# Performance work log

Measured on AMD Instinct MI355X. Metric: run time of the kernel, lower is better.

## Reference

```python
import math
import jax, jax.numpy as jnp
import numpy as np

IN_SIZE = 1024
OUT_SIZE = 1024
LOG_N = 10          # ceil(log2(in_size))
NSTACKS = 1         # ceil(out_size / 2**LOG_N)
NBLOCKS = 1


def setup_inputs() -> dict:
    key = jax.random.key(0)
    k1, k2, k3 = jax.random.split(key, 3)
    x = jax.random.normal(k1, (8, 4096, IN_SIZE), dtype=jnp.float32)
    # twiddle init: randn * 1/sqrt(2)  (ortho_init=False, real)
    twiddle = jax.random.normal(
        k2, (NSTACKS, NBLOCKS, LOG_N, IN_SIZE // 2, 2, 2), dtype=jnp.float32
    ) * (1.0 / math.sqrt(2.0))
    bound = 1.0 / math.sqrt(IN_SIZE)
    bias = jax.random.uniform(k3, (OUT_SIZE,), minval=-bound, maxval=bound,
                              dtype=jnp.float32)
    return {"x": x, "twiddle": twiddle, "bias": bias}


def butterfly_multiply(twiddle, x, increasing_stride=True):
    """twiddle: (nstacks, nblocks, log_n, n/2, 2, 2); x: (batch, nstacks, n)."""
    b, nstacks, n = x.shape
    nblocks, log_n = twiddle.shape[1], twiddle.shape[2]
    out = x
    inc = increasing_stride
    for blk in range(nblocks):
        for idx in range(log_n):
            log_stride = idx if inc else log_n - 1 - idx
            stride = 1 << log_stride
            # t: (nstacks, n/(2*stride), stride, 2, 2)
            t = twiddle[:, blk, idx].reshape(nstacks, n // (2 * stride), stride, 2, 2)
            # o: (batch, nstacks, n/(2*stride), 2, stride)
            o = out.reshape(b, nstacks, n // (2 * stride), 2, stride)
            # 2x2 rotation applied across pairs separated by `stride`
            out = jnp.einsum('sgrij,bsgjr->bsgir', t, o).reshape(b, nstacks, n)
        inc = not inc
    return out


def reference(x, twiddle, bias):
    batch_shape = x.shape[:-1]
    xf = x.reshape(-1, IN_SIZE)                       # pre_process (no pad: 1024=2**10)
    xb = jnp.broadcast_to(xf[:, None, :], (xf.shape[0], NSTACKS, IN_SIZE))
    out = butterfly_multiply(twiddle, xb, increasing_stride=True)
    out = out.reshape(xf.shape[0], NSTACKS * IN_SIZE)[:, :OUT_SIZE]
    out = out + bias
    return out.reshape(*batch_shape, OUT_SIZE)
```

## Files before the change

kernel.cpp:

```cpp
#include <hip/hip_runtime.h>


#define ROWS_PER_WAVE 4
#define N 1024

__global__ __launch_bounds__(256) void permute_tw_kernel(
    const float* __restrict__ tw, float* __restrict__ ws)
{
    const int s = blockIdx.x;
    const int t = threadIdx.x;
    #pragma unroll
    for (int it = 0; it < 8; ++it) {
        const int g = it * 256 + t;
        const float val = tw[s * 2048 + g];
        int dst;
        if (s < 4) {
            const int l  = g >> 5;
            const int r  = g & 31;
            dst = (r >> 2) * 256 + l * 4 + (r & 3);
        } else {
            const int p  = g >> 2;
            const int c  = g & 3;
            const int i  = c >> 1;
            const int j  = c & 1;
            const int pl = p >> 4;
            const int k  = p & 15;
            const int lm = s - 4;
            const int m  = 1 << lm;
            const int l  = ((pl >> lm) << (lm + 1)) | (i << lm) | (pl & (m - 1));
            dst = (k >> 1) * 256 + l * 4 + (k & 1) * 2 + (j ^ i);
        }
        ws[s * 2048 + dst] = val;
    }
}

__global__ __launch_bounds__(256, 4) void butterfly_kernel(
    const float* __restrict__ x,
    const float* __restrict__ ws,
    const float* __restrict__ bias,
    float* __restrict__ out,
    int nRows)
{
    const int lane = threadIdx.x & 63;
    const int waveInBlock = threadIdx.x >> 6;
    const int waveId = blockIdx.x * 4 + waveInBlock;
    const long rowBase = (long)waveId * ROWS_PER_WAVE;
    if (rowBase >= nRows) return;

    const int off = lane * 16;

    float v[ROWS_PER_WAVE][16];

    #pragma unroll
    for (int r = 0; r < ROWS_PER_WAVE; ++r) {
        const float4* p = (const float4*)(x + (rowBase + r) * N + off);
        #pragma unroll
        for (int q = 0; q < 4; ++q) {
            float4 f = p[q];
            v[r][q*4+0] = f.x; v[r][q*4+1] = f.y;
            v[r][q*4+2] = f.z; v[r][q*4+3] = f.w;
        }
    }

    #pragma unroll
    for (int stage = 0; stage < 4; ++stage) {
        const int s = 1 << stage;
        float t[32];
        const float4* tp = (const float4*)(ws + stage * 2048) + lane;
        #pragma unroll
        for (int q = 0; q < 8; ++q) {
            float4 f = tp[q * 64];
            t[q*4+0] = f.x; t[q*4+1] = f.y; t[q*4+2] = f.z; t[q*4+3] = f.w;
        }
        #pragma unroll
        for (int r = 0; r < ROWS_PER_WAVE; ++r) {
            #pragma unroll
            for (int j = 0; j < 8; ++j) {
                const int p0 = ((j >> stage) << (stage + 1)) | (j & (s - 1));
                const int p1 = p0 | s;
                float a = v[r][p0], b = v[r][p1];
                v[r][p0] = t[j*4+0] * a + t[j*4+1] * b;
                v[r][p1] = t[j*4+2] * a + t[j*4+3] * b;
            }
        }
    }

    #pragma unroll
    for (int stage = 4; stage < 10; ++stage) {
        const int m = 1 << (stage - 4);
        float ta_[16], tb_[16];
        const float4* tp = (const float4*)(ws + stage * 2048) + lane;
        #pragma unroll
        for (int kk = 0; kk < 8; ++kk) {
            float4 f = tp[kk * 64];
            ta_[2*kk+0] = f.x; tb_[2*kk+0] = f.y;
            ta_[2*kk+1] = f.z; tb_[2*kk+1] = f.w;
        }
        #pragma unroll
        for (int r = 0; r < ROWS_PER_WAVE; ++r) {
            #pragma unroll
            for (int k = 0; k < 16; ++k) {
                float mine  = v[r][k];
                float other = __shfl_xor(mine, m, 64);
                v[r][k] = ta_[k] * mine + tb_[k] * other;
            }
        }
    }

    float bv[16];
    {
        const float4* bp = (const float4*)(bias + off);
        #pragma unroll
        for (int q = 0; q < 4; ++q) {
            float4 f = bp[q];
            bv[q*4+0] = f.x; bv[q*4+1] = f.y;
            bv[q*4+2] = f.z; bv[q*4+3] = f.w;
        }
    }
    #pragma unroll
    for (int r = 0; r < ROWS_PER_WAVE; ++r) {
        float4* p = (float4*)(out + (rowBase + r) * N + off);
        #pragma unroll
        for (int q = 0; q < 4; ++q) {
            float4 f;
            f.x = v[r][q*4+0] + bv[q*4+0];
            f.y = v[r][q*4+1] + bv[q*4+1];
            f.z = v[r][q*4+2] + bv[q*4+2];
            f.w = v[r][q*4+3] + bv[q*4+3];
            p[q] = f;
        }
    }
}

extern "C" void kernel_launch(void* const* d_in, const int* in_sizes, int n_in,
                              void* d_out, int out_size, void* d_ws, size_t ws_size,
                              hipStream_t stream) {
    const float* x    = (const float*)d_in[0];
    const float* tw   = (const float*)d_in[1];
    const float* bias = (const float*)d_in[2];
    float* out = (float*)d_out;
    float* ws  = (float*)d_ws;

    permute_tw_kernel<<<10, 256, 0, stream>>>(tw, ws);

    const int nRows = in_sizes[0] / N;
    const int waves = (nRows + ROWS_PER_WAVE - 1) / ROWS_PER_WAVE;
    const int blocks = (waves + 3) / 4;

    butterfly_kernel<<<blocks, 256, 0, stream>>>(x, ws, bias, out, nRows);
}
```

Baseline: 299.5 us.

## Stage twiddles in LDS, software-pipeline row loads, use ds_swizzle for exchanges

Each block copies the permuted twiddles for nine stages into dynamic shared memory, and the last stage still reads from global memory. Each wave handles eight rows in pairs, with double-buffered register loads so the next rows' global reads overlap the current butterfly compute. Lane exchanges with xor distance below 32 use ds_swizzle instead of shfl_xor. The aim is to cut repeated global twiddle traffic and hide memory latency. The costs are a 72KB LDS footprint per block, which limits occupancy, a per-block copy cost, and the risk that twiddle reads are now bound by LDS bandwidth.

After: 880.2 us. 194% more time.

```diff
diff --git a/kernel.cpp b/kernel.cpp
--- a/kernel.cpp
+++ b/kernel.cpp
@@ -1,8 +1,11 @@
 #include <hip/hip_runtime.h>
 
 
-#define ROWS_PER_WAVE 4
 #define N 1024
+#define BLOCK_THREADS 512
+#define WAVES_PER_BLOCK 8
+#define ROWS_PER_WAVE 8
+#define LDS_STAGES 9
 
 __global__ __launch_bounds__(256) void permute_tw_kernel(
     const float* __restrict__ tw, float* __restrict__ ws)
@@ -34,101 +37,166 @@
     }
 }
 
-__global__ __launch_bounds__(256, 4) void butterfly_kernel(
+template<int M>
+__device__ __forceinline__ float sx(float v) {
+    if constexpr (M < 32) {
+        return __int_as_float(__builtin_amdgcn_ds_swizzle(
+            __float_as_int(v), (M << 10) | 0x1f));
+    } else {
+        return __shfl_xor(v, 32, 64);
+    }
+}
+
+__device__ __forceinline__ void loadRow(float (&v)[16],
+                                        const float* __restrict__ x,
+                                        long row, int off)
+{
+    const float4* p = (const float4*)(x + row * N + off);
+    #pragma unroll
+    for (int q = 0; q < 4; ++q) {
+        float4 f = p[q];
+        v[q*4+0] = f.x; v[q*4+1] = f.y;
+        v[q*4+2] = f.z; v[q*4+3] = f.w;
+    }
+}
+
+__device__ __forceinline__ void computeStore(
+    float (&v0)[16], float (&v1)[16],
+    const float* ldsTw,
+    const float* __restrict__ ws,
+    const float* __restrict__ bias,
+    float* __restrict__ out,
+    long row, int lane, int nRows)
+{
+    const int off = lane * 16;
+
+    #pragma unroll
+    for (int stage = 0; stage < 4; ++stage) {
+        const int s = 1 << stage;
+        float t[32];
+        const float4* tp = (const float4*)(ldsTw + stage * 2048) + lane;
+        #pragma unroll
+        for (int q = 0; q < 8; ++q) {
+            float4 f = tp[q * 64];
+            t[q*4+0] = f.x; t[q*4+1] = f.y; t[q*4+2] = f.z; t[q*4+3] = f.w;
+        }
+        #pragma unroll
+        for (int j = 0; j < 8; ++j) {
+            const int p0 = ((j >> stage) << (stage + 1)) | (j & (s - 1));
+            const int p1 = p0 | s;
+            { float a = v0[p0], b = v0[p1];
+              v0[p0] = t[j*4+0]*a + t[j*4+1]*b;
+              v0[p1] = t[j*4+2]*a + t[j*4+3]*b; }
+            { float a = v1[p0], b = v1[p1];
+              v1[p0] = t[j*4+0]*a + t[j*4+1]*b;
+              v1[p1] = t[j*4+2]*a + t[j*4+3]*b; }
+        }
+    }
+
+#define XSTAGE(STG, BASEPTR) { \
+    constexpr int M = 1 << ((STG) - 4); \
+    float ta_[16], tb_[16]; \
+    const float4* tp = (const float4*)((BASEPTR) + (STG) * 2048) + lane; \
+    _Pragma("unroll") \
+    for (int kk = 0; kk < 8; ++kk) { \
+        float4 f = tp[kk * 64]; \
+        ta_[2*kk+0] = f.x; tb_[2*kk+0] = f.y; \
+        ta_[2*kk+1] = f.z; tb_[2*kk+1] = f.w; } \
+    _Pragma("unroll") \
+    for (int k = 0; k < 16; ++k) { \
+        float m0 = v0[k], o0 = sx<M>(m0); \
+        float m1 = v1[k], o1 = sx<M>(m1); \
+        v0[k] = ta_[k]*m0 + tb_[k]*o0; \
+        v1[k] = ta_[k]*m1 + tb_[k]*o1; } \
+}
+    XSTAGE(4, ldsTw)
+    XSTAGE(5, ldsTw)
+    XSTAGE(6, ldsTw)
+    XSTAGE(7, ldsTw)
+    XSTAGE(8, ldsTw)
+    XSTAGE(9, ws)
+#undef XSTAGE
+
+    float bv[16];
+    {
+        const float4* bp = (const float4*)(bias + off);
+        #pragma unroll
+        for (int q = 0; q < 4; ++q) {
+            float4 f = bp[q];
+            bv[q*4+0] = f.x; bv[q*4+1] = f.y;
+            bv[q*4+2] = f.z; bv[q*4+3] = f.w;
+        }
+    }
+    if (row < nRows) {
+        float4* p = (float4*)(out + row * N + off);
+        #pragma unroll
+        for (int q = 0; q < 4; ++q) {
+            float4 f;
+            f.x = v0[q*4+0] + bv[q*4+0];
+            f.y = v0[q*4+1] + bv[q*4+1];
+            f.z = v0[q*4+2] + bv[q*4+2];
+            f.w = v0[q*4+3] + bv[q*4+3];
+            p[q] = f;
+        }
+    }
+    if (row + 1 < nRows) {
+        float4* p = (float4*)(out + (row + 1) * N + off);
+        #pragma unroll
+        for (int q = 0; q < 4; ++q) {
+            float4 f;
+            f.x = v1[q*4+0] + bv[q*4+0];
+            f.y = v1[q*4+1] + bv[q*4+1];
+            f.z = v1[q*4+2] + bv[q*4+2];
+            f.w = v1[q*4+3] + bv[q*4+3];
+            p[q] = f;
+        }
+    }
+}
+
+__global__ __launch_bounds__(BLOCK_THREADS, 4) void butterfly_kernel(
     const float* __restrict__ x,
     const float* __restrict__ ws,
     const float* __restrict__ bias,
     float* __restrict__ out,
     int nRows)
 {
+    extern __shared__ float ldsTw[];
+
+    {
+        const int t = threadIdx.x;
+        const float4* src = (const float4*)ws;
+        float4* dst = (float4*)ldsTw;
+        #pragma unroll
+        for (int i = 0; i < (LDS_STAGES * 2048 / 4) / BLOCK_THREADS; ++i)
+            dst[i * BLOCK_THREADS + t] = src[i * BLOCK_THREADS + t];
+    }
+    __syncthreads();
+
     const int lane = threadIdx.x & 63;
-    const int waveInBlock = threadIdx.x >> 6;
-    const int waveId = blockIdx.x * 4 + waveInBlock;
+    const int off = lane * 16;
+    const int waveId = blockIdx.x * WAVES_PER_BLOCK + (threadIdx.x >> 6);
     const long rowBase = (long)waveId * ROWS_PER_WAVE;
     if (rowBase >= nRows) return;
 
-    const int off = lane * 16;
-
-    float v[ROWS_PER_WAVE][16];
-
-    #pragma unroll
-    for (int r = 0; r < ROWS_PER_WAVE; ++r) {
-        const float4* p = (const float4*)(x + (rowBase + r) * N + off);
-        #pragma unroll
-        for (int q = 0; q < 4; ++q) {
-            float4 f = p[q];
-            v[r][q*4+0] = f.x; v[r][q*4+1] = f.y;
-            v[r][q*4+2] = f.z; v[r][q*4+3] = f.w;
-        }
-    }
-
-    #pragma unroll
-    for (int stage = 0; stage < 4; ++stage) {
-        const int s = 1 << stage;
-        float t[32];
-        const float4* tp = (const float4*)(ws + stage * 2048) + lane;
-        #pragma unroll
-        for (int q = 0; q < 8; ++q) {
-            float4 f = tp[q * 64];
-            t[q*4+0] = f.x; t[q*4+1] = f.y; t[q*4+2] = f.z; t[q*4+3] = f.w;
-        }
-        #pragma unroll
-        for (int r = 0; r < ROWS_PER_WAVE; ++r) {
-            #pragma unroll
-            for (int j = 0; j < 8; ++j) {
-                const int p0 = ((j >> stage) << (stage + 1)) | (j & (s - 1));
-                const int p1 = p0 | s;
-                float a = v[r][p0], b = v[r][p1];
-                v[r][p0] = t[j*4+0] * a + t[j*4+1] * b;
-                v[r][p1] = t[j*4+2] * a + t[j*4+3] * b;
-            }
-        }
-    }
-
-    #pragma unroll
-    for (int stage = 4; stage < 10; ++stage) {
-        const int m = 1 << (stage - 4);
-        float ta_[16], tb_[16];
-        const float4* tp = (const float4*)(ws + stage * 2048) + lane;
-        #pragma unroll
-        for (int kk = 0; kk < 8; ++kk) {
-            float4 f = tp[kk * 64];
-            ta_[2*kk+0] = f.x; tb_[2*kk+0] = f.y;
-            ta_[2*kk+1] = f.z; tb_[2*kk+1] = f.w;
-        }
-        #pragma unroll
-        for (int r = 0; r < ROWS_PER_WAVE; ++r) {
-            #pragma unroll
-            for (int k = 0; k < 16; ++k) {
-                float mine  = v[r][k];
-                float other = __shfl_xor(mine, m, 64);
-                v[r][k] = ta_[k] * mine + tb_[k] * other;
-            }
-        }
-    }
-
-    float bv[16];
-    {
-        const float4* bp = (const float4*)(bias + off);
-        #pragma unroll
-        for (int q = 0; q < 4; ++q) {
-            float4 f = bp[q];
-            bv[q*4+0] = f.x; bv[q*4+1] = f.y;
-            bv[q*4+2] = f.z; bv[q*4+3] = f.w;
-        }
-    }
-    #pragma unroll
-    for (int r = 0; r < ROWS_PER_WAVE; ++r) {
-        float4* p = (float4*)(out + (rowBase + r) * N + off);
-        #pragma unroll
-        for (int q = 0; q < 4; ++q) {
-            float4 f;
-            f.x = v[r][q*4+0] + bv[q*4+0];
-            f.y = v[r][q*4+1] + bv[q*4+1];
-            f.z = v[r][q*4+2] + bv[q*4+2];
-            f.w = v[r][q*4+3] + bv[q*4+3];
-            p[q] = f;
-        }
+    float A0[16], A1[16], B0[16], B1[16];
+
+    auto clampRow = [&](long r) { return r < nRows ? r : rowBase; };
+
+    loadRow(A0, x, rowBase, off);
+    loadRow(A1, x, clampRow(rowBase + 1), off);
+
+    long r = rowBase;
+    #pragma unroll 1
+    for (int it = 0; it < 2; ++it) {
+        loadRow(B0, x, clampRow(r + 2), off);
+        loadRow(B1, x, clampRow(r + 3), off);
+        computeStore(A0, A1, ldsTw, ws, bias, out, r, lane, nRows);
+        if (it == 0) {
+            loadRow(A0, x, clampRow(r + 4), off);
+            loadRow(A1, x, clampRow(r + 5), off);
+        }
+        computeStore(B0, B1, ldsTw, ws, bias, out, r + 2, lane, nRows);
+        r += 4;
     }
 }
 
@@ -141,11 +209,21 @@
     float* out = (float*)d_out;
     float* ws  = (float*)d_ws;
 
+    const size_t ldsBytes = (size_t)LDS_STAGES * 2048 * sizeof(float);
+    static bool attrSet = false;
+    if (!attrSet) {
+        hipFuncSetAttribute((const void*)butterfly_kernel,
+                            hipFuncAttributeMaxDynamicSharedMemorySize,
+                            (int)ldsBytes);
+        attrSet = true;
+    }
+
     permute_tw_kernel<<<10, 256, 0, stream>>>(tw, ws);
 
     const int nRows = in_sizes[0] / N;
-    const int waves = (nRows + ROWS_PER_WAVE - 1) / ROWS_PER_WAVE;
-    const int blocks = (waves + 3) / 4;
-
-    butterfly_kernel<<<blocks, 256, 0, stream>>>(x, ws, bias, out, nRows);
-}
+    const int rowsPerBlock = WAVES_PER_BLOCK * ROWS_PER_WAVE;
+    const int blocks = (nRows + rowsPerBlock - 1) / rowsPerBlock;
+
+    butterfly_kernel<<<blocks, BLOCK_THREADS, ldsBytes, stream>>>(
+        x, ws, bias, out, nRows);
+}
```

## Stage twiddles in LDS, use ds_swizzle for cross-lane exchanges, widen blocks

Applied to the files above, without the earlier changes.

Each block first copies all ten permuted twiddle stages (80 KB) into shared memory, and the butterfly stages then read twiddles from LDS instead of global memory. Cross-lane exchanges with xor distance below 32 now use ds_swizzle instead of the generic shuffle. Blocks grow to 512 threads so the LDS fill is shared across 8 waves. Every block now pays for an 80 KB copy plus a barrier, and the large LDS footprint limits how many blocks fit per CU, which can cut occupancy on this memory-bound kernel.

New measurement: 267.3 us. 1.12x faster.

```diff
diff --git a/kernel.cpp b/kernel.cpp
--- a/kernel.cpp
+++ b/kernel.cpp
@@ -1,8 +1,11 @@
 #include <hip/hip_runtime.h>
 
 
+#define N 1024
+#define BLOCK_THREADS 512
+#define WAVES_PER_BLOCK 8
 #define ROWS_PER_WAVE 4
-#define N 1024
+#define NSTAGES 10
 
 __global__ __launch_bounds__(256) void permute_tw_kernel(
     const float* __restrict__ tw, float* __restrict__ ws)
@@ -34,20 +37,40 @@
     }
 }
 
-__global__ __launch_bounds__(256, 4) void butterfly_kernel(
+template<int M>
+__device__ __forceinline__ float sx(float v) {
+    if constexpr (M < 32) {
+        return __int_as_float(__builtin_amdgcn_ds_swizzle(
+            __float_as_int(v), (M << 10) | 0x1f));
+    } else {
+        return __shfl_xor(v, 32, 64);
+    }
+}
+
+__global__ __launch_bounds__(BLOCK_THREADS) void butterfly_kernel(
     const float* __restrict__ x,
     const float* __restrict__ ws,
     const float* __restrict__ bias,
     float* __restrict__ out,
     int nRows)
 {
+    extern __shared__ float ldsTw[];
+
+    {
+        const int t = threadIdx.x;
+        const float4* src = (const float4*)ws;
+        float4* dst = (float4*)ldsTw;
+        #pragma unroll
+        for (int i = 0; i < (NSTAGES * 2048 / 4) / BLOCK_THREADS; ++i)
+            dst[i * BLOCK_THREADS + t] = src[i * BLOCK_THREADS + t];
+    }
+    __syncthreads();
+
     const int lane = threadIdx.x & 63;
-    const int waveInBlock = threadIdx.x >> 6;
-    const int waveId = blockIdx.x * 4 + waveInBlock;
+    const int off = lane * 16;
+    const int waveId = blockIdx.x * WAVES_PER_BLOCK + (threadIdx.x >> 6);
     const long rowBase = (long)waveId * ROWS_PER_WAVE;
     if (rowBase >= nRows) return;
-
-    const int off = lane * 16;
 
     float v[ROWS_PER_WAVE][16];
 
@@ -66,7 +89,7 @@
     for (int stage = 0; stage < 4; ++stage) {
         const int s = 1 << stage;
         float t[32];
-        const float4* tp = (const float4*)(ws + stage * 2048) + lane;
+        const float4* tp = (const float4*)(ldsTw + stage * 2048) + lane;
         #pragma unroll
         for (int q = 0; q < 8; ++q) {
             float4 f = tp[q * 64];
@@ -85,27 +108,30 @@
         }
     }
 
-    #pragma unroll
-    for (int stage = 4; stage < 10; ++stage) {
-        const int m = 1 << (stage - 4);
-        float ta_[16], tb_[16];
-        const float4* tp = (const float4*)(ws + stage * 2048) + lane;
-        #pragma unroll
-        for (int kk = 0; kk < 8; ++kk) {
-            float4 f = tp[kk * 64];
-            ta_[2*kk+0] = f.x; tb_[2*kk+0] = f.y;
-            ta_[2*kk+1] = f.z; tb_[2*kk+1] = f.w;
-        }
-        #pragma unroll
-        for (int r = 0; r < ROWS_PER_WAVE; ++r) {
-            #pragma unroll
-            for (int k = 0; k < 16; ++k) {
-                float mine  = v[r][k];
-                float other = __shfl_xor(mine, m, 64);
-                v[r][k] = ta_[k] * mine + tb_[k] * other;
-            }
-        }
-    }
+#define XSTAGE(STG) { \
+    constexpr int M = 1 << ((STG) - 4); \
+    float ta_[16], tb_[16]; \
+    const float4* tp = (const float4*)(ldsTw + (STG) * 2048) + lane; \
+    _Pragma("unroll") \
+    for (int kk = 0; kk < 8; ++kk) { \
+        float4 f = tp[kk * 64]; \
+        ta_[2*kk+0] = f.x; tb_[2*kk+0] = f.y; \
+        ta_[2*kk+1] = f.z; tb_[2*kk+1] = f.w; } \
+    _Pragma("unroll") \
+    for (int r = 0; r < ROWS_PER_WAVE; ++r) { \
+        _Pragma("unroll") \
+        for (int k = 0; k < 16; ++k) { \
+            float mine  = v[r][k]; \
+            float other = sx<M>(mine); \
+            v[r][k] = ta_[k] * mine + tb_[k] * other; } } \
+}
+    XSTAGE(4)
+    XSTAGE(5)
+    XSTAGE(6)
+    XSTAGE(7)
+    XSTAGE(8)
+    XSTAGE(9)
+#undef XSTAGE
 
     float bv[16];
     {
@@ -141,11 +167,21 @@
     float* out = (float*)d_out;
     float* ws  = (float*)d_ws;
 
+    const size_t ldsBytes = (size_t)NSTAGES * 2048 * sizeof(float);
+    static bool attrSet = false;
+    if (!attrSet) {
+        hipFuncSetAttribute((const void*)butterfly_kernel,
+                            hipFuncAttributeMaxDynamicSharedMemorySize,
+                            (int)ldsBytes);
+        attrSet = true;
+    }
+
     permute_tw_kernel<<<10, 256, 0, stream>>>(tw, ws);
 
     const int nRows = in_sizes[0] / N;
-    const int waves = (nRows + ROWS_PER_WAVE - 1) / ROWS_PER_WAVE;
-    const int blocks = (waves + 3) / 4;
+    const int rowsPerBlock = WAVES_PER_BLOCK * ROWS_PER_WAVE;
+    const int blocks = (nRows + rowsPerBlock - 1) / rowsPerBlock;
 
-    butterfly_kernel<<<blocks, 256, 0, stream>>>(x, ws, bias, out, nRows);
+    butterfly_kernel<<<blocks, BLOCK_THREADS, ldsBytes, stream>>>(
+        x, ws, bias, out, nRows);
 }
```
